# Kernel tuning notes

Measured on AMD Instinct MI355X. Metric: run time of the kernel, lower is better.

## Reference

```python
import jax, jax.numpy as jnp
import numpy as np

EMBED_DIM = 1024
NUM_HEADS = 16
HEAD_DIM = EMBED_DIM // NUM_HEADS  # 64


def setup_inputs() -> dict:
    key = jax.random.key(0)
    ks = jax.random.split(key, 9)
    B, S, D, Hd = 2, 2048, EMBED_DIM, HEAD_DIM
    s_in = 1.0 / np.sqrt(D)
    s_out = 1.0 / np.sqrt(D)
    return {
        "x": jax.random.normal(ks[0], (B, S, D), dtype=jnp.float32),
        # weights stored [in, out] (transpose of torch Linear.weight)
        "wq": jax.random.uniform(ks[1], (D, D), jnp.float32, -s_in, s_in),
        "bq": jax.random.uniform(ks[2], (D,), jnp.float32, -s_in, s_in),
        "wk": jax.random.uniform(ks[3], (D, Hd), jnp.float32, -s_in, s_in),
        "bk": jax.random.uniform(ks[4], (Hd,), jnp.float32, -s_in, s_in),
        "wv": jax.random.uniform(ks[5], (D, Hd), jnp.float32, -s_in, s_in),
        "bv": jax.random.uniform(ks[6], (Hd,), jnp.float32, -s_in, s_in),
        "wo": jax.random.uniform(ks[7], (D, D), jnp.float32, -s_out, s_out),
        "bo": jax.random.uniform(ks[8], (D,), jnp.float32, -s_out, s_out),
    }


def reference(x, wq, bq, wk, bk, wv, bv, wo, bo):
    B, S, D = x.shape
    H, Hd = NUM_HEADS, HEAD_DIM
    q = (x @ wq + bq).reshape(B, S, H, Hd)  # per-head queries
    k = x @ wk + bk                          # shared single-head keys  [B,S,Hd]
    v = x @ wv + bv                          # shared single-head values [B,S,Hd]
    # NOTE: original scales by embed_dim**-0.5 (not head_dim) — keep faithful.
    scores = jnp.einsum('bqhd,bkd->bhqk', q, k) / jnp.sqrt(jnp.float32(D))
    attn = jax.nn.softmax(scores, axis=-1)
    out = jnp.einsum('bhqk,bkd->bqhd', attn, v).reshape(B, S, D)
    return out @ wo + bo
```

## Files before the change

### kernel.cpp

```cpp
#include <hip/hip_runtime.h>

typedef unsigned short ushort_t;
typedef __attribute__((ext_vector_type(8))) short short8;
typedef __attribute__((ext_vector_type(4))) float f32x4;

#define EMBED 1024
#define NHEADS 16
#define HDIM 64
#define SEQ 2048
#define BATCH 2
#define BS (BATCH*SEQ)
#define QSCALE 0.045084234f

static __device__ __forceinline__ ushort_t f2b(float x) {
    union { float f; unsigned u; } v; v.f = x;
    unsigned r = v.u + 0x7FFFu + ((v.u >> 16) & 1u);
    return (ushort_t)(r >> 16);
}

static __device__ __forceinline__ void gload_lds16(const void* g, void* l) {
    __builtin_amdgcn_global_load_lds(
        (const __attribute__((address_space(1))) void*)g,
        (__attribute__((address_space(3))) void*)l, 16, 0, 0);
}

static __device__ __forceinline__ float exp2_raw(float x) {
    float r;
    asm("v_exp_f32 %0, %1" : "=v"(r) : "v"(x));
    return r;
}

__global__ __launch_bounds__(256) void prep_kernel(
    const float* __restrict__ x,
    const float* __restrict__ wq, const float* __restrict__ wk,
    const float* __restrict__ wv, const float* __restrict__ wo,
    ushort_t* __restrict__ xb, ushort_t* __restrict__ wqkv_t,
    ushort_t* __restrict__ wo_t)
{
    __shared__ float LsT[64][65];
    const int bid = blockIdx.x;
    const int t = threadIdx.x;

    if (bid < 2048) {
        const size_t i = ((size_t)bid * 256 + t) * 8;
        float4 f0 = *reinterpret_cast<const float4*>(x + i);
        float4 f1 = *reinterpret_cast<const float4*>(x + i + 4);
        short8 h;
        h[0] = (short)f2b(f0.x); h[1] = (short)f2b(f0.y);
        h[2] = (short)f2b(f0.z); h[3] = (short)f2b(f0.w);
        h[4] = (short)f2b(f1.x); h[5] = (short)f2b(f1.y);
        h[6] = (short)f2b(f1.z); h[7] = (short)f2b(f1.w);
        *reinterpret_cast<short8*>(xb + i) = h;
        return;
    }

    const float* src; ushort_t* dst; int N, bx, by;
    if (bid < 2304)      { int r = bid - 2048; src = wq; dst = wqkv_t;            N = 1024; bx = r & 15; by = r >> 4; }
    else if (bid < 2320) { int r = bid - 2304; src = wk; dst = wqkv_t + 1024*1024; N = 64;  bx = 0;      by = r; }
    else if (bid < 2336) { int r = bid - 2320; src = wv; dst = wqkv_t + 1088*1024; N = 64;  bx = 0;      by = r; }
    else                 { int r = bid - 2336; src = wo; dst = wo_t;              N = 1024; bx = r & 15; by = r >> 4; }
    const int n0 = bx * 64, k0 = by * 64;
    const int rr0 = t >> 4;
    const int c4 = (t & 15) * 4;
    #pragma unroll
    for (int rr = 0; rr < 4; ++rr) {
        float4 f = *reinterpret_cast<const float4*>(
            src + (size_t)(k0 + rr0 + rr * 16) * N + n0 + c4);
        LsT[c4 + 0][rr0 + rr * 16] = f.x;
        LsT[c4 + 1][rr0 + rr * 16] = f.y;
        LsT[c4 + 2][rr0 + rr * 16] = f.z;
        LsT[c4 + 3][rr0 + rr * 16] = f.w;
    }
    __syncthreads();
    const int rn = t >> 2;
    const int c16 = (t & 3) * 16;
    ushort_t* d = dst + (size_t)(n0 + rn) * 1024 + k0 + c16;
    short8 h0, h1;
    #pragma unroll
    for (int i = 0; i < 8; ++i) h0[i] = (short)f2b(LsT[rn][c16 + i]);
    #pragma unroll
    for (int i = 0; i < 8; ++i) h1[i] = (short)f2b(LsT[rn][c16 + 8 + i]);
    *reinterpret_cast<short8*>(d) = h0;
    *reinterpret_cast<short8*>(d + 8) = h1;
}

template<int MODE, int NWGX>
__global__ __launch_bounds__(256, 3) void mfma_gemm(
    const ushort_t* __restrict__ A, const ushort_t* __restrict__ Bt,
    const float* __restrict__ b0, const float* __restrict__ b1,
    const float* __restrict__ b2,
    float* __restrict__ Of, ushort_t* __restrict__ Oq,
    ushort_t* __restrict__ Okb, ushort_t* __restrict__ Ovt)
{
    __shared__ char smem[49152];

    const int tid = threadIdx.x;
    const int lane = tid & 63;
    const int w = tid >> 6;
    const int g = lane >> 4;
    const int c = lane & 15;

    const int bidl = blockIdx.y * NWGX + blockIdx.x;
    const int cpx = (NWGX * 32) >> 3;
    const int swz = (bidl & 7) * cpx + (bidl >> 3);
    const int rowBase = (swz / NWGX) * 128;
    const int colBase = (swz % NWGX) * 64;

    const int lr = lane >> 3;
    const int so = ((lane & 7) * 16) ^ (lr << 4);

    const char* Abase = (const char*)A + (size_t)rowBase * 2048;
    const char* Bbase = (const char*)Bt + (size_t)colBase * 2048;

    f32x4 acc[2][4];
    #pragma unroll
    for (int i = 0; i < 2; ++i)
        #pragma unroll
        for (int j = 0; j < 4; ++j)
            acc[i][j] = (f32x4){0.f, 0.f, 0.f, 0.f};

    #define STAGE(step, buf) do {                                              \
        char* T_ = smem + (buf) * 24576;                                       \
        const size_t kb_ = (size_t)(step) * 128;                               \
        _Pragma("unroll")                                                      \
        for (int u = 0; u < 4; ++u) {                                          \
            const int ca = 4 * w + u;                                          \
            gload_lds16(Abase + (size_t)(ca * 8 + lr) * 2048 + kb_ + so,       \
                        T_ + ca * 1024);                                       \
        }                                                                      \
        _Pragma("unroll")                                                      \
        for (int u = 0; u < 2; ++u) {                                          \
            const int cb = 2 * w + u;                                          \
            gload_lds16(Bbase + (size_t)(cb * 8 + lr) * 2048 + kb_ + so,       \
                        T_ + 16384 + cb * 1024);                               \
        }                                                                      \
    } while (0)

    STAGE(0, 0);
    __syncthreads();

    for (int i = 0; i < 16; ++i) {
        const int cur = i & 1;
        if (i < 15) STAGE(i + 1, cur ^ 1);

        const char* As = smem + cur * 24576;
        const char* Bs = As + 16384;
        #pragma unroll
        for (int ks = 0; ks < 2; ++ks) {
            short8 af[2], bf[4];
            #pragma unroll
            for (int mt = 0; mt < 2; ++mt) {
                const int row = w * 32 + mt * 16 + c;
                af[mt] = *reinterpret_cast<const short8*>(
                    As + row * 128 + ((ks * 64 + g * 16) ^ ((row & 7) << 4)));
            }
            #pragma unroll
            for (int nt = 0; nt < 4; ++nt) {
                const int row = nt * 16 + c;
                bf[nt] = *reinterpret_cast<const short8*>(
                    Bs + row * 128 + ((ks * 64 + g * 16) ^ ((row & 7) << 4)));
            }
            #pragma unroll
            for (int mt = 0; mt < 2; ++mt)
                #pragma unroll
                for (int nt = 0; nt < 4; ++nt)
                    acc[mt][nt] = __builtin_amdgcn_mfma_f32_16x16x32_bf16(
                        af[mt], bf[nt], acc[mt][nt], 0, 0, 0);
        }

        __syncthreads();
    }
    #undef STAGE

    #pragma unroll
    for (int nt = 0; nt < 4; ++nt) {
        const int colAbs = colBase + nt * 16 + c;
        #pragma unroll
        for (int mt = 0; mt < 2; ++mt) {
            const int rowA = rowBase + w * 32 + mt * 16 + g * 4;
            #pragma unroll
            for (int r = 0; r < 4; ++r) {
                const float v = acc[mt][nt][r];
                const int row = rowA + r;
                if (MODE == 2) {
                    Of[(size_t)row * 1024 + colAbs] = v + b0[colAbs];
                } else {
                    if (colAbs < 1024) {
                        Oq[(size_t)row * 1024 + colAbs] = f2b((v + b0[colAbs]) * QSCALE);
                    } else if (colAbs < 1088) {
                        const int kc = colAbs - 1024;
                        Okb[(size_t)row * 64 + kc] = f2b(v + b1[kc]);
                    } else {
                        const int hd = colAbs - 1088;
                        const int bb = row >> 11, s = row & 2047;
                        const int key = s & 63;
                        const int pos = (key & 0x23) | ((key & 0x0C) << 1) | ((key & 0x10) >> 2);
                        Ovt[((((size_t)bb * 32 + (s >> 6)) * 4 + (hd >> 4)) * 16
                             + (hd & 15)) * 64 + pos] = f2b(v + b2[hd]);
                    }
                }
            }
        }
    }
}

#define PSWZ(row, kbyte) ((row) * 128 + ((kbyte) ^ (((row) & 7) << 4)))

__global__ __launch_bounds__(512, 4) void attn_mfma_kernel(
    const ushort_t* __restrict__ q,
    const ushort_t* __restrict__ kb,
    const ushort_t* __restrict__ vt,
    ushort_t* __restrict__ aout)
{
    __shared__ char smem[65536];
    char* Ks0 = smem;
    char* Ks1 = smem + 16384;
    char* Vs0 = smem + 32768;
    char* Vs1 = smem + 49152;

    const int tid = threadIdx.x;
    const int lane = tid & 63;
    const int w = tid >> 6;
    const int g = lane >> 4;
    const int c = lane & 15;
    const int bid = blockIdx.x;
    const int qt = bid & 31;
    const int hp = (bid >> 5) & 7;
    const int b = bid >> 8;
    const int q0 = qt * 64;
    const int h = hp * 2 + (w >> 2);
    const int wq = w & 3;

    short8 bq[2];
    {
        const size_t qrow = (size_t)(b * SEQ + q0 + wq * 16 + c) * 1024 + h * 64;
        bq[0] = *reinterpret_cast<const short8*>(q + qrow + g * 8);
        bq[1] = *reinterpret_cast<const short8*>(q + qrow + 32 + g * 8);
    }

    short8 vone;
    #pragma unroll
    for (int i = 0; i < 8; ++i) vone[i] = (short)0x3F80;

    const char* kbb = (const char*)kb + (size_t)b * SEQ * 128;
    const char* vbb = (const char*)vt + (size_t)b * 262144;

    const int lr = lane >> 3;
    const int so = ((lane & 7) * 16) ^ (lr << 4);

    f32x4 oacc[4];
    #pragma unroll
    for (int i = 0; i < 4; ++i) oacc[i] = (f32x4){0.f, 0.f, 0.f, 0.f};
    f32x4 lacc = (f32x4){0.f, 0.f, 0.f, 0.f};

    #pragma unroll
    for (int u = 0; u < 4; ++u) {
        const int ch = w * 4 + u;
        const int cc = ch & 15;
        const size_t srcoff = (size_t)(cc * 8 + lr) * 128 + so;
        if (ch < 16) gload_lds16(kbb + srcoff, Ks0 + cc * 1024);
        else         gload_lds16(vbb + srcoff, Vs0 + cc * 1024);
    }
    __syncthreads();

    const int csw = (c & 7) << 4;

    union U { unsigned u[4]; short8 s8; };

    for (int kt = 0; kt < SEQ / 128; ++kt) {
        char* ksb = (kt & 1) ? Ks1 : Ks0;
        char* vsb = (kt & 1) ? Vs1 : Vs0;
        char* ksn = (kt & 1) ? Ks0 : Ks1;
        char* vsn = (kt & 1) ? Vs0 : Vs1;

        {
            const int ktn = (kt < SEQ / 128 - 1) ? kt + 1 : kt;
            const char* gKt = kbb + (size_t)ktn * 16384;
            const char* gVt = vbb + (size_t)ktn * 16384;
            #pragma unroll
            for (int u = 0; u < 4; ++u) {
                const int ch = w * 4 + u;
                const int cc = ch & 15;
                const size_t srcoff = (size_t)(cc * 8 + lr) * 128 + so;
                if (ch < 16) gload_lds16(gKt + srcoff, ksn + cc * 1024);
                else         gload_lds16(gVt + srcoff, vsn + cc * 1024);
            }
        }

        f32x4 sacc0[4], sacc1[4];
        __builtin_amdgcn_s_setprio(1);
        #pragma unroll
        for (int mt = 0; mt < 4; ++mt) {
            const char* kr = ksb + (mt * 16 + c) * 128;
            short8 k0 = *reinterpret_cast<const short8*>(kr + ((g * 16) ^ csw));
            short8 k1 = *reinterpret_cast<const short8*>(kr + ((64 + g * 16) ^ csw));
            f32x4 z = (f32x4){0.f, 0.f, 0.f, 0.f};
            z = __builtin_amdgcn_mfma_f32_16x16x32_bf16(k0, bq[0], z, 0, 0, 0);
            z = __builtin_amdgcn_mfma_f32_16x16x32_bf16(k1, bq[1], z, 0, 0, 0);
            sacc0[mt] = z;
        }
        #pragma unroll
        for (int mt = 0; mt < 4; ++mt) {
            const char* kr = ksb + 8192 + (mt * 16 + c) * 128;
            short8 k0 = *reinterpret_cast<const short8*>(kr + ((g * 16) ^ csw));
            short8 k1 = *reinterpret_cast<const short8*>(kr + ((64 + g * 16) ^ csw));
            f32x4 z = (f32x4){0.f, 0.f, 0.f, 0.f};
            z = __builtin_amdgcn_mfma_f32_16x16x32_bf16(k0, bq[0], z, 0, 0, 0);
            z = __builtin_amdgcn_mfma_f32_16x16x32_bf16(k1, bq[1], z, 0, 0, 0);
            sacc1[mt] = z;
        }
        __builtin_amdgcn_s_setprio(0);

        U pa0[2], pa1[2];
        {
            float pe[4][4];
            #pragma unroll
            for (int mt = 0; mt < 4; ++mt)
                #pragma unroll
                for (int r = 0; r < 4; ++r)
                    pe[mt][r] = exp2_raw(sacc0[mt][r]);
            #pragma unroll
            for (int ks = 0; ks < 2; ++ks) {
                asm("v_cvt_pk_bf16_f32 %0, %1, %2" : "=v"(pa0[ks].u[0])
                    : "v"(pe[2*ks][0]), "v"(pe[2*ks][1]));
                asm("v_cvt_pk_bf16_f32 %0, %1, %2" : "=v"(pa0[ks].u[1])
                    : "v"(pe[2*ks][2]), "v"(pe[2*ks][3]));
                asm("v_cvt_pk_bf16_f32 %0, %1, %2" : "=v"(pa0[ks].u[2])
                    : "v"(pe[2*ks+1][0]), "v"(pe[2*ks+1][1]));
                asm("v_cvt_pk_bf16_f32 %0, %1, %2" : "=v"(pa0[ks].u[3])
                    : "v"(pe[2*ks+1][2]), "v"(pe[2*ks+1][3]));
            }
        }
        {
            float pe[4][4];
            #pragma unroll
            for (int mt = 0; mt < 4; ++mt)
                #pragma unroll
                for (int r = 0; r < 4; ++r)
                    pe[mt][r] = exp2_raw(sacc1[mt][r]);
            #pragma unroll
            for (int ks = 0; ks < 2; ++ks) {
                asm("v_cvt_pk_bf16_f32 %0, %1, %2" : "=v"(pa1[ks].u[0])
                    : "v"(pe[2*ks][0]), "v"(pe[2*ks][1]));
                asm("v_cvt_pk_bf16_f32 %0, %1, %2" : "=v"(pa1[ks].u[1])
                    : "v"(pe[2*ks][2]), "v"(pe[2*ks][3]));
                asm("v_cvt_pk_bf16_f32 %0, %1, %2" : "=v"(pa1[ks].u[2])
                    : "v"(pe[2*ks+1][0]), "v"(pe[2*ks+1][1]));
                asm("v_cvt_pk_bf16_f32 %0, %1, %2" : "=v"(pa1[ks].u[3])
                    : "v"(pe[2*ks+1][2]), "v"(pe[2*ks+1][3]));
            }
        }

        __builtin_amdgcn_s_setprio(1);
        #pragma unroll
        for (int ks = 0; ks < 2; ++ks) {
            #pragma unroll
            for (int nt = 0; nt < 4; ++nt) {
                short8 vf = *reinterpret_cast<const short8*>(
                    vsb + (nt * 16 + c) * 128 + ((ks * 64 + g * 16) ^ csw));
                oacc[nt] = __builtin_amdgcn_mfma_f32_16x16x32_bf16(
                    pa0[ks].s8, vf, oacc[nt], 0, 0, 0);
            }
            lacc = __builtin_amdgcn_mfma_f32_16x16x32_bf16(
                pa0[ks].s8, vone, lacc, 0, 0, 0);
        }
        #pragma unroll
        for (int ks = 0; ks < 2; ++ks) {
            #pragma unroll
            for (int nt = 0; nt < 4; ++nt) {
                short8 vf = *reinterpret_cast<const short8*>(
                    vsb + 8192 + (nt * 16 + c) * 128 + ((ks * 64 + g * 16) ^ csw));
                oacc[nt] = __builtin_amdgcn_mfma_f32_16x16x32_bf16(
                    pa1[ks].s8, vf, oacc[nt], 0, 0, 0);
            }
            lacc = __builtin_amdgcn_mfma_f32_16x16x32_bf16(
                pa1[ks].s8, vone, lacc, 0, 0, 0);
        }
        __builtin_amdgcn_s_setprio(0);

        __syncthreads();
    }

    float linv[4];
    #pragma unroll
    for (int r = 0; r < 4; ++r) linv[r] = 1.0f / lacc[r];
    char* escr = smem + (w << 11);
    #pragma unroll
    for (int nt = 0; nt < 4; ++nt)
        #pragma unroll
        for (int r = 0; r < 4; ++r)
            *reinterpret_cast<ushort_t*>(escr + PSWZ(g * 4 + r, (nt * 16 + c) * 2)) =
                f2b(oacc[nt][r] * linv[r]);
    {
        const int qr = lane >> 2, ch = lane & 3;
        uint4 d0 = *reinterpret_cast<const uint4*>(escr + PSWZ(qr, ch * 32));
        uint4 d1 = *reinterpret_cast<const uint4*>(escr + PSWZ(qr, ch * 32 + 16));
        ushort_t* dst = aout + (size_t)(b * SEQ + q0 + wq * 16 + qr) * 1024 + h * 64 + ch * 16;
        *reinterpret_cast<uint4*>(dst) = d0;
        *reinterpret_cast<uint4*>(dst + 8) = d1;
    }
}

extern "C" void kernel_launch(void* const* d_in, const int* in_sizes, int n_in,
                              void* d_out, int out_size, void* d_ws, size_t ws_size,
                              hipStream_t stream) {
    const float* x  = (const float*)d_in[0];
    const float* wq = (const float*)d_in[1];
    const float* bq = (const float*)d_in[2];
    const float* wk = (const float*)d_in[3];
    const float* bk = (const float*)d_in[4];
    const float* wv = (const float*)d_in[5];
    const float* bv = (const float*)d_in[6];
    const float* wo = (const float*)d_in[7];
    const float* bo = (const float*)d_in[8];
    float* out = (float*)d_out;

    ushort_t* ws     = (ushort_t*)d_ws;
    ushort_t* wqkv_t = ws;
    ushort_t* wo_t   = wqkv_t + 1152 * 1024;
    ushort_t* kbuf   = wo_t + 1024 * 1024;
    ushort_t* vtb    = kbuf + (size_t)BS * 64;
    ushort_t* qabuf  = vtb + (size_t)BS * 64;
    ushort_t* xb     = (ushort_t*)d_out;

    prep_kernel<<<2592, 256, 0, stream>>>(x, wq, wk, wv, wo, xb, wqkv_t, wo_t);

    mfma_gemm<0, 18><<<dim3(18, 32), 256, 0, stream>>>(xb, wqkv_t, bq, bk, bv,
                                                       nullptr, qabuf, kbuf, vtb);
    attn_mfma_kernel<<<BATCH * (NHEADS / 2) * (SEQ / 64), 512, 0, stream>>>(
        qabuf, kbuf, vtb, qabuf);
    mfma_gemm<2, 16><<<dim3(16, 32), 256, 0, stream>>>(qabuf, wo_t, bo, nullptr, nullptr,
                                                       out, nullptr, nullptr, nullptr);
}
```

Measured before the change: 85.74 us.

## Split attention key range in two with separate reduction kernel

Attention is split into two halves along the key dimension. This doubles the grid from 512 to 1024 blocks and lets each block run half the key tiles, with exponentials computed without running-max rescaling. Each half writes unnormalized bf16 partial outputs and row sums to workspace, and a new reduce kernel adds the halves and normalizes. The cost is an extra launch, extra global traffic for the partials, and bf16 rounding of the partial sums. The split path runs only if the workspace is large enough; otherwise the old kernel is used.

```diff
diff --git a/kernel.cpp b/kernel.cpp
--- a/kernel.cpp
+++ b/kernel.cpp
@@ -16,6 +16,12 @@
     union { float f; unsigned u; } v; v.f = x;
     unsigned r = v.u + 0x7FFFu + ((v.u >> 16) & 1u);
     return (ushort_t)(r >> 16);
+}
+
+static __device__ __forceinline__ float b2f(short v) {
+    union { unsigned u; float f; } z;
+    z.u = ((unsigned)(unsigned short)v) << 16;
+    return z.f;
 }
 
 static __device__ __forceinline__ void gload_lds16(const void* g, void* l) {
@@ -401,6 +407,175 @@
     }
 }
 
+__global__ __launch_bounds__(512, 6) void attn_splitk_kernel(
+    const ushort_t* __restrict__ q,
+    const ushort_t* __restrict__ kb,
+    const ushort_t* __restrict__ vt,
+    ushort_t* __restrict__ pout,
+    float* __restrict__ lbuf)
+{
+    __shared__ char smem[32768];
+    char* Ks0 = smem;
+    char* Ks1 = smem + 8192;
+    char* Vs0 = smem + 16384;
+    char* Vs1 = smem + 24576;
+
+    const int tid = threadIdx.x;
+    const int lane = tid & 63;
+    const int w = tid >> 6;
+    const int g = lane >> 4;
+    const int c = lane & 15;
+    const int bid = blockIdx.x;
+    const int qt = bid & 31;
+    const int hp = (bid >> 5) & 7;
+    const int b = (bid >> 8) & 1;
+    const int kh = bid >> 9;
+    const int q0 = qt * 64;
+    const int h = hp * 2 + (w >> 2);
+    const int wq = w & 3;
+
+    short8 bq[2];
+    {
+        const size_t qrow = (size_t)(b * SEQ + q0 + wq * 16 + c) * 1024 + h * 64;
+        bq[0] = *reinterpret_cast<const short8*>(q + qrow + g * 8);
+        bq[1] = *reinterpret_cast<const short8*>(q + qrow + 32 + g * 8);
+    }
+
+    short8 vone;
+    #pragma unroll
+    for (int i = 0; i < 8; ++i) vone[i] = (short)0x3F80;
+
+    const char* kbb = (const char*)kb + (size_t)b * SEQ * 128 + (size_t)kh * 131072;
+    const char* vbb = (const char*)vt + (size_t)b * 262144 + (size_t)kh * 131072;
+
+    const int lr = lane >> 3;
+    const int so = ((lane & 7) * 16) ^ (lr << 4);
+    const int csw = (c & 7) << 4;
+
+    f32x4 oacc[4];
+    #pragma unroll
+    for (int i = 0; i < 4; ++i) oacc[i] = (f32x4){0.f, 0.f, 0.f, 0.f};
+    f32x4 lacc = (f32x4){0.f, 0.f, 0.f, 0.f};
+
+    #define STG64(t, kd, vd) do {                                              \
+        _Pragma("unroll")                                                      \
+        for (int u = 0; u < 2; ++u) {                                          \
+            const int ch = w * 2 + u;                               \
+            const int cc = ch & 7;                                             \
+            const size_t srcoff = (size_t)(t) * 8192 + (cc * 8 + lr) * 128 + so; \
+            if (ch < 8) gload_lds16(kbb + srcoff, (kd) + cc * 1024);           \
+            else        gload_lds16(vbb + srcoff, (vd) + cc * 1024);           \
+        }                                                                      \
+    } while (0)
+
+    STG64(0, Ks0, Vs0);
+    __syncthreads();
+
+    union U { unsigned u[4]; short8 s8; };
+
+    for (int kt = 0; kt < 16; ++kt) {
+        char* ksb = (kt & 1) ? Ks1 : Ks0;
+        char* vsb = (kt & 1) ? Vs1 : Vs0;
+        char* ksn = (kt & 1) ? Ks0 : Ks1;
+        char* vsn = (kt & 1) ? Vs0 : Vs1;
+
+        const int ktn = (kt < 15) ? kt + 1 : kt;
+        STG64(ktn, ksn, vsn);
+
+        f32x4 sacc[4];
+        __builtin_amdgcn_s_setprio(1);
+        #pragma unroll
+        for (int mt = 0; mt < 4; ++mt) {
+            const char* kr = ksb + (mt * 16 + c) * 128;
+            short8 k0 = *reinterpret_cast<const short8*>(kr + ((g * 16) ^ csw));
+            short8 k1 = *reinterpret_cast<const short8*>(kr + ((64 + g * 16) ^ csw));
+            f32x4 z = (f32x4){0.f, 0.f, 0.f, 0.f};
+            z = __builtin_amdgcn_mfma_f32_16x16x32_bf16(k0, bq[0], z, 0, 0, 0);
+            z = __builtin_amdgcn_mfma_f32_16x16x32_bf16(k1, bq[1], z, 0, 0, 0);
+            sacc[mt] = z;
+        }
+        __builtin_amdgcn_s_setprio(0);
+
+        float pe[4][4];
+        #pragma unroll
+        for (int mt = 0; mt < 4; ++mt)
+            #pragma unroll
+            for (int r = 0; r < 4; ++r)
+                pe[mt][r] = exp2_raw(sacc[mt][r]);
+
+        U pa[2];
+        #pragma unroll
+        for (int ks = 0; ks < 2; ++ks) {
+            asm("v_cvt_pk_bf16_f32 %0, %1, %2" : "=v"(pa[ks].u[0])
+                : "v"(pe[2*ks][0]), "v"(pe[2*ks][1]));
+            asm("v_cvt_pk_bf16_f32 %0, %1, %2" : "=v"(pa[ks].u[1])
+                : "v"(pe[2*ks][2]), "v"(pe[2*ks][3]));
+            asm("v_cvt_pk_bf16_f32 %0, %1, %2" : "=v"(pa[ks].u[2])
+                : "v"(pe[2*ks+1][0]), "v"(pe[2*ks+1][1]));
+            asm("v_cvt_pk_bf16_f32 %0, %1, %2" : "=v"(pa[ks].u[3])
+                : "v"(pe[2*ks+1][2]), "v"(pe[2*ks+1][3]));
+        }
+
+        __builtin_amdgcn_s_setprio(1);
+        #pragma unroll
+        for (int ks = 0; ks < 2; ++ks) {
+            #pragma unroll
+            for (int nt = 0; nt < 4; ++nt) {
+                short8 vf = *reinterpret_cast<const short8*>(
+                    vsb + (nt * 16 + c) * 128 + ((ks * 64 + g * 16) ^ csw));
+                oacc[nt] = __builtin_amdgcn_mfma_f32_16x16x32_bf16(
+                    pa[ks].s8, vf, oacc[nt], 0, 0, 0);
+            }
+            lacc = __builtin_amdgcn_mfma_f32_16x16x32_bf16(
+                pa[ks].s8, vone, lacc, 0, 0, 0);
+        }
+        __builtin_amdgcn_s_setprio(0);
+
+        __syncthreads();
+    }
+    #undef STG64
+
+    if (c == 0) {
+        #pragma unroll
+        for (int r = 0; r < 4; ++r)
+            lbuf[(size_t)kh * 65536 +
+                 (size_t)(b * SEQ + q0 + wq * 16 + g * 4 + r) * 16 + h] = lacc[r];
+    }
+    char* escr = smem + (w << 11);
+    #pragma unroll
+    for (int nt = 0; nt < 4; ++nt)
+        #pragma unroll
+        for (int r = 0; r < 4; ++r)
+            *reinterpret_cast<ushort_t*>(escr + PSWZ(g * 4 + r, (nt * 16 + c) * 2)) =
+                f2b(oacc[nt][r]);
+    {
+        const int qr = lane >> 2, ch = lane & 3;
+        uint4 d0 = *reinterpret_cast<const uint4*>(escr + PSWZ(qr, ch * 32));
+        uint4 d1 = *reinterpret_cast<const uint4*>(escr + PSWZ(qr, ch * 32 + 16));
+        ushort_t* dst = pout + (size_t)kh * 4194304 +
+                        (size_t)(b * SEQ + q0 + wq * 16 + qr) * 1024 + h * 64 + ch * 16;
+        *reinterpret_cast<uint4*>(dst) = d0;
+        *reinterpret_cast<uint4*>(dst + 8) = d1;
+    }
+}
+
+__global__ __launch_bounds__(256) void attn_reduce_kernel(
+    const ushort_t* __restrict__ pout, const float* __restrict__ lbuf,
+    ushort_t* __restrict__ aout)
+{
+    const size_t i = ((size_t)blockIdx.x * 256 + threadIdx.x) * 8;
+    const int row = (int)(i >> 10);
+    const int head = ((int)i & 1023) >> 6;
+    const float inv = 1.0f / (lbuf[row * 16 + head] + lbuf[65536 + row * 16 + head]);
+    short8 p0 = *reinterpret_cast<const short8*>(pout + i);
+    short8 p1 = *reinterpret_cast<const short8*>(pout + 4194304 + i);
+    short8 o;
+    #pragma unroll
+    for (int j = 0; j < 8; ++j)
+        o[j] = (short)f2b((b2f(p0[j]) + b2f(p1[j])) * inv);
+    *reinterpret_cast<short8*>(aout + i) = o;
+}
+
 extern "C" void kernel_launch(void* const* d_in, const int* in_sizes, int n_in,
                               void* d_out, int out_size, void* d_ws, size_t ws_size,
                               hipStream_t stream) {
@@ -421,14 +596,23 @@
     ushort_t* kbuf   = wo_t + 1024 * 1024;
     ushort_t* vtb    = kbuf + (size_t)BS * 64;
     ushort_t* qabuf  = vtb + (size_t)BS * 64;
+    ushort_t* pout   = qabuf + (size_t)BS * 1024;
+    float*    lbuf   = (float*)(pout + (size_t)2 * BS * 1024);
     ushort_t* xb     = (ushort_t*)d_out;
 
     prep_kernel<<<2592, 256, 0, stream>>>(x, wq, wk, wv, wo, xb, wqkv_t, wo_t);
 
     mfma_gemm<0, 18><<<dim3(18, 32), 256, 0, stream>>>(xb, wqkv_t, bq, bk, bv,
                                                        nullptr, qabuf, kbuf, vtb);
-    attn_mfma_kernel<<<BATCH * (NHEADS / 2) * (SEQ / 64), 512, 0, stream>>>(
-        qabuf, kbuf, vtb, qabuf);
+    const size_t ws_need = (size_t)(6946816 + 8388608) * 2 + 524288;
+    if (ws_size >= ws_need) {
+        attn_splitk_kernel<<<2 * BATCH * (NHEADS / 2) * (SEQ / 64), 512, 0, stream>>>(
+            qabuf, kbuf, vtb, pout, lbuf);
+        attn_reduce_kernel<<<(BS * 1024) / 8 / 256, 256, 0, stream>>>(pout, lbuf, qabuf);
+    } else {
+        attn_mfma_kernel<<<BATCH * (NHEADS / 2) * (SEQ / 64), 512, 0, stream>>>(
+            qabuf, kbuf, vtb, qabuf);
+    }
     mfma_gemm<2, 16><<<dim3(16, 32), 256, 0, stream>>>(qabuf, wo_t, bo, nullptr, nullptr,
                                                        out, nullptr, nullptr, nullptr);
 }
```

After: 92.34 us. +7.7%, slower.
